# Performance work log

Measured on AMD Instinct MI355X. Metric: run time of the kernel, lower is better.

The kernel has to match this reference:

```python
import jax, jax.numpy as jnp
import numpy as np

B, S, D, H, F = 2, 2048, 768, 12, 3072
DH = D // H  # head dim = 64


def setup_inputs() -> dict:
    key = jax.random.key(0)
    ks = jax.random.split(key, 16)
    sc = 0.02
    p = {
        "src": jax.random.normal(ks[0], (B, S, D), jnp.float32),
        # attention projections (torch Linear layout: [out, in], bias=True in xformers MultiHeadDispatch)
        "wq": jax.random.normal(ks[1], (D, D), jnp.float32) * sc,
        "bq": jnp.zeros((D,), jnp.float32),
        "wk": jax.random.normal(ks[2], (D, D), jnp.float32) * sc,
        "bk": jnp.zeros((D,), jnp.float32),
        "wv": jax.random.normal(ks[3], (D, D), jnp.float32) * sc,
        "bv": jnp.zeros((D,), jnp.float32),
        "wo": jax.random.normal(ks[4], (D, D), jnp.float32) * sc,
        "bo": jnp.zeros((D,), jnp.float32),
        # FFN: fc1 (bias) -> SwiGLU (two bias-free F->F projections) -> fc2 (bias)
        "w_fc1": jax.random.normal(ks[5], (F, D), jnp.float32) * sc,
        "b_fc1": jnp.zeros((F,), jnp.float32),
        "w_in": jax.random.normal(ks[6], (F, F), jnp.float32) * sc,
        "w_gate": jax.random.normal(ks[7], (F, F), jnp.float32) * sc,
        "w_fc2": jax.random.normal(ks[8], (D, F), jnp.float32) * sc,
        "b_fc2": jnp.zeros((D,), jnp.float32),
        # RMSNorm weights
        "g_attn": jnp.ones((D,), jnp.float32),
        "g_ffn": jnp.ones((D,), jnp.float32),
    }
    return p


def _rmsnorm(x, g):
    eps = jnp.asarray(jnp.finfo(x.dtype).eps, x.dtype)
    return x * jax.lax.rsqrt(jnp.mean(x * x, axis=-1, keepdims=True) + eps) * g


def _rope_cos_sin(seq_len, dim, dtype):
    # xformers RotaryEmbedding: inv_freq over even indices, emb = cat(freqs, freqs)
    inv_freq = 1.0 / (10000.0 ** (jnp.arange(0, dim, 2, dtype=jnp.float32) / dim))
    freqs = jnp.arange(seq_len, dtype=jnp.float32)[:, None] * inv_freq[None, :]  # [S, dim/2]
    emb = jnp.concatenate([freqs, freqs], axis=-1)  # [S, dim]
    return jnp.cos(emb).astype(dtype), jnp.sin(emb).astype(dtype)


def _rotate_half(x):
    x1, x2 = jnp.split(x, 2, axis=-1)
    return jnp.concatenate([-x2, x1], axis=-1)


def _apply_rope(x, cos, sin):
    # x: [B, H, S, DH]; cos/sin: [S, DH]
    return x * cos[None, None] + _rotate_half(x) * sin[None, None]


def _block(src, wq, bq, wk, bk, wv, bv, wo, bo,
           w_fc1, b_fc1, w_in, w_gate, w_fc2, b_fc2, g_attn, g_ffn):
    b, s, d = src.shape
    x = _rmsnorm(src, g_attn)
    q = (x @ wq.T + bq).reshape(b, s, H, DH).transpose(0, 2, 1, 3)
    k = (x @ wk.T + bk).reshape(b, s, H, DH).transpose(0, 2, 1, 3)
    v = (x @ wv.T + bv).reshape(b, s, H, DH).transpose(0, 2, 1, 3)
    cos, sin = _rope_cos_sin(s, DH, x.dtype)
    q = _apply_rope(q, cos, sin)
    k = _apply_rope(k, cos, sin)
    scale = 1.0 / np.sqrt(DH)
    scores = jnp.einsum("bhsd,bhtd->bhst", q * scale, k)  # non-causal, no mask
    attn = jax.nn.softmax(scores, axis=-1)
    ctx = jnp.einsum("bhst,bhtd->bhsd", attn, v)
    ctx = ctx.transpose(0, 2, 1, 3).reshape(b, s, d)
    attn_out = ctx @ wo.T + bo

    y = _rmsnorm(src + attn_out, g_ffn)
    h = y @ w_fc1.T + b_fc1
    h = (h @ w_in.T) * jax.nn.silu(h @ w_gate.T)  # SwiGLU
    ffn_out = h @ w_fc2.T + b_fc2
    return y + ffn_out


def reference(src, wq, bq, wk, bk, wv, bv, wo, bo,
              w_fc1, b_fc1, w_in, w_gate, w_fc2, b_fc2, g_attn, g_ffn):
    return _block(src, wq, bq, wk, bk, wv, bv, wo, bo,
                  w_fc1, b_fc1, w_in, w_gate, w_fc2, b_fc2, g_attn, g_ffn)
```

## Files before the change

### kernel.cpp

```cpp
#include <hip/hip_runtime.h>

#define DEV static __device__ __forceinline__

typedef __attribute__((ext_vector_type(8))) short bf16x8;
typedef __attribute__((ext_vector_type(4))) short short4v;
typedef __attribute__((ext_vector_type(4))) float f32x4;

DEV f32x4 mfma16(bf16x8 a, bf16x8 b, f32x4 c){
  return __builtin_amdgcn_mfma_f32_16x16x32_bf16(a, b, c, 0, 0, 0);
}
DEV float bf2f(short s){ union{unsigned u; float f;} v; v.u=((unsigned)(unsigned short)s)<<16; return v.f; }
DEV short f2bf(float f){ union{float f; unsigned u;} v; v.f=f; unsigned r=v.u+0x7fffu+((v.u>>16)&1u); return (short)(r>>16); }
DEV void gload16(const void* g, void* l){
  __builtin_amdgcn_global_load_lds((const __attribute__((address_space(1))) void*)g,
                                   (__attribute__((address_space(3))) void*)l, 16, 0, 0);
}
DEV int cvtpk(float lo, float hi){
  int r; asm("v_cvt_pk_bf16_f32 %0, %1, %2" : "=v"(r) : "v"(lo), "v"(hi)); return r;
}

enum { EPI_BF16=0, EPI_RESID=2, EPI_QKV=4 };

__global__ void k_convert7(const float* __restrict__ p0, const float* __restrict__ p1,
                           const float* __restrict__ p2, const float* __restrict__ p3,
                           const float* __restrict__ p4, const float* __restrict__ p5,
                           const float* __restrict__ p6, short* __restrict__ dst){
  int v = blockIdx.x * 256 + threadIdx.x;
  const float* src; int rel;
  if      (v <  147456){ src=p0; rel=v; }
  else if (v <  294912){ src=p1; rel=v-147456; }
  else if (v <  442368){ src=p2; rel=v-294912; }
  else if (v <  589824){ src=p3; rel=v-442368; }
  else if (v < 2949120){ src=p4; rel=v-589824; }
  else if (v < 5308416){ src=p5; rel=v-2949120; }
  else                 { src=p6; rel=v-5308416; }
  float4 x = ((const float4*)src)[rel];
  short4v o; o.x=f2bf(x.x); o.y=f2bf(x.y); o.z=f2bf(x.z); o.w=f2bf(x.w);
  int dv = (v < 589824) ? v : (v + 589824);
  ((short4v*)dst)[dv] = o;
}

__global__ void k_convertT(const float* __restrict__ in, short* __restrict__ out){
  __shared__ float lt[32][33];
  const int t = threadIdx.x;
  const int f0 = blockIdx.x * 32;
  const int d0 = blockIdx.y * 32;
  int r = t >> 3, c4 = t & 7;
  float4 v = *(const float4*)(in + (size_t)(f0 + r)*768 + d0 + c4*4);
  lt[r][c4*4+0] = v.x; lt[r][c4*4+1] = v.y; lt[r][c4*4+2] = v.z; lt[r][c4*4+3] = v.w;
  __syncthreads();
  short4v o;
  o.x = f2bf(lt[c4*4+0][r]);
  o.y = f2bf(lt[c4*4+1][r]);
  o.z = f2bf(lt[c4*4+2][r]);
  o.w = f2bf(lt[c4*4+3][r]);
  *(short4v*)(out + (size_t)(d0 + r)*3072 + f0 + c4*4) = o;
}

__global__ void k_gemv(const short* __restrict__ W, const float* __restrict__ b,
                       float* __restrict__ out){
  int row = blockIdx.x*4 + (threadIdx.x>>6);
  int lane = threadIdx.x & 63;
  const short* wr = W + (size_t)row*3072 + lane*48;
  const float* bb = b + lane*48;
  float s = 0.f;
  #pragma unroll
  for (int i=0;i<6;i++){
    bf16x8 w = *(const bf16x8*)(wr + i*8);
    float4 b0 = *(const float4*)(bb + i*8);
    float4 b1 = *(const float4*)(bb + i*8 + 4);
    s += bf2f(w[0])*b0.x + bf2f(w[1])*b0.y + bf2f(w[2])*b0.z + bf2f(w[3])*b0.w
       + bf2f(w[4])*b1.x + bf2f(w[5])*b1.y + bf2f(w[6])*b1.z + bf2f(w[7])*b1.w;
  }
  #pragma unroll
  for (int d=32; d>0; d>>=1) s += __shfl_xor(s, d);
  if (lane == 0) out[row] = s;
}

__global__ void k_rmsnorm(const float* __restrict__ x, const float* __restrict__ g,
                          short* __restrict__ out){
  int row = blockIdx.x*4 + (threadIdx.x>>6);
  int lane = threadIdx.x & 63;
  const float* xr = x + (size_t)row*768;
  float4 v[3];
  float ss = 0.f;
  #pragma unroll
  for (int i=0;i<3;i++){
    v[i] = *(const float4*)(xr + i*256 + lane*4);
    ss += v[i].x*v[i].x + v[i].y*v[i].y + v[i].z*v[i].z + v[i].w*v[i].w;
  }
  #pragma unroll
  for (int d=32; d>0; d>>=1) ss += __shfl_xor(ss, d);
  float sc = rsqrtf(ss*(1.f/768.f) + 1.1920929e-7f);
  #pragma unroll
  for (int i=0;i<3;i++){
    int c0 = i*256 + lane*4;
    float4 gv = *(const float4*)(g + c0);
    short4v o;
    o.x = f2bf(v[i].x*sc*gv.x); o.y = f2bf(v[i].y*sc*gv.y);
    o.z = f2bf(v[i].z*sc*gv.z); o.w = f2bf(v[i].w*sc*gv.w);
    *(short4v*)(out + (size_t)row*768 + c0) = o;
  }
}

template<int EPI>
__launch_bounds__(256, 2)
__global__ void k_gemm(const short* __restrict__ Aptr, const short* __restrict__ Bptr,
                       void* __restrict__ Cout, const float* __restrict__ bias,
                       const void* __restrict__ aux, const float* __restrict__ bias2,
                       const float* __restrict__ bias3, const void* __restrict__ aux2,
                       int M, int N, int K){
  __shared__ short ldsA[128*32];
  __shared__ short ldsB[128*32];
  const int t = threadIdx.x;
  const int wave = t >> 6, lane = t & 63;
  const int l15 = lane & 15, l4 = lane >> 4;
  const int nwg = gridDim.x * gridDim.y;
  const int bid0 = blockIdx.y * gridDim.x + blockIdx.x;
  const int cpx = nwg >> 3;
  const int bid = (bid0 & 7) * cpx + (bid0 >> 3);
  const int bm = bid / gridDim.x, bn = bid % gridDim.x;
  const int wr = wave >> 1, wc = wave & 1;

  f32x4 acc[4][4] = {};

  const short* Ag = Aptr + (size_t)(bm*128 + wave*32 + (lane>>2))*K + (lane&3)*8;
  const short* Bg = Bptr + (size_t)(bn*128 + wave*32 + (lane>>2))*K + (lane&3)*8;
  short* lA = ldsA + wave*1024;
  short* lB = ldsB + wave*1024;

  for (int k0 = 0; k0 < K; k0 += 32){
    __syncthreads();
    gload16(Ag + k0,                lA);
    gload16(Ag + k0 + 16*(size_t)K, lA + 512);
    gload16(Bg + k0,                lB);
    gload16(Bg + k0 + 16*(size_t)K, lB + 512);
    __syncthreads();
    bf16x8 af[4], bfr[4];
    #pragma unroll
    for (int m=0;m<4;m++) af[m]  = *(const bf16x8*)(ldsA + (wr*64 + m*16 + l15)*32 + l4*8);
    #pragma unroll
    for (int n=0;n<4;n++) bfr[n] = *(const bf16x8*)(ldsB + (wc*64 + n*16 + l15)*32 + l4*8);
    #pragma unroll
    for (int m=0;m<4;m++)
      #pragma unroll
      for (int n=0;n<4;n++)
        acc[m][n] = mfma16(af[m], bfr[n], acc[m][n]);
  }

  const int row0 = bm*128 + wr*64;
  const int col0 = bn*128 + wc*64;

  if constexpr (EPI == EPI_BF16){
    short* C = (short*)Cout;
    #pragma unroll
    for (int m=0;m<4;m++)
      #pragma unroll
      for (int j=0;j<4;j++){
        size_t rb = (size_t)(row0 + m*16 + l4*4 + j)*N + col0 + l15;
        #pragma unroll
        for (int n=0;n<4;n++) C[rb + n*16] = f2bf(acc[m][n][j]);
      }
  } else if constexpr (EPI == EPI_RESID){
    float* C = (float*)Cout;
    const float* srcf = (const float*)aux;
    float bvv[4];
    #pragma unroll
    for (int n=0;n<4;n++) bvv[n] = bias[col0 + n*16 + l15];
    #pragma unroll
    for (int m=0;m<4;m++)
      #pragma unroll
      for (int j=0;j<4;j++){
        size_t rb = (size_t)(row0 + m*16 + l4*4 + j)*N + col0 + l15;
        #pragma unroll
        for (int n=0;n<4;n++) C[rb + n*16] = acc[m][n][j] + bvv[n] + srcf[rb + n*16];
      }
  } else if constexpr (EPI == EPI_QKV){
    const int proj = col0 / 768;
    const int c768 = col0 - proj*768;
    const int h = c768 >> 6;
    const float* bs = proj==0 ? bias : (proj==1 ? bias2 : bias3);
    float bvv[4];
    #pragma unroll
    for (int n=0;n<4;n++) bvv[n] = bs[c768 + n*16 + l15];
    if (proj == 2){
      short* Ov = (short*)const_cast<void*>(aux2);
      #pragma unroll
      for (int m=0;m<4;m++){
        #pragma unroll
        for (int j=0;j<4;j++){
          int row = row0 + m*16 + l4*4 + j;
          int b = row >> 11, s = row & 2047;
          size_t hb = (size_t)(b*12 + h)*64;
          #pragma unroll
          for (int n=0;n<4;n++)
            Ov[(hb + n*16 + l15)*2048 + s] = f2bf(acc[m][n][j] + bvv[n]);
        }
      }
    } else {
      short* O = proj==0 ? (short*)Cout : (short*)const_cast<void*>(aux);
      const float sc = proj==0 ? 0.18033688011112042f : 1.0f;
      const float RC = 0.41524101186092034f;
      float invf0 = exp2f(-(float)l15 * RC);
      float invf1 = exp2f(-(float)(16 + l15) * RC);
      #pragma unroll
      for (int m=0;m<4;m++){
        #pragma unroll
        for (int j=0;j<4;j++){
          int row = row0 + m*16 + l4*4 + j;
          int b = row >> 11, s = row & 2047;
          size_t obase = ((size_t)(b*12 + h)*2048 + (size_t)s)*64;
          float a0 = acc[m][0][j] + bvv[0];
          float a1 = acc[m][1][j] + bvv[1];
          float a2 = acc[m][2][j] + bvv[2];
          float a3 = acc[m][3][j] + bvv[3];
          float sn0, cs0, sn1, cs1;
          __sincosf((float)s * invf0, &sn0, &cs0);
          __sincosf((float)s * invf1, &sn1, &cs1);
          O[obase + l15]      = f2bf((a0*cs0 - a2*sn0)*sc);
          O[obase + 16 + l15] = f2bf((a1*cs1 - a3*sn1)*sc);
          O[obase + 32 + l15] = f2bf((a2*cs0 + a0*sn0)*sc);
          O[obase + 48 + l15] = f2bf((a3*cs1 + a1*sn1)*sc);
        }
      }
    }
  }
}

__launch_bounds__(256, 2)
__global__ void k_wpart(const short* __restrict__ Aptr, const short* __restrict__ Bptr,
                        short* __restrict__ P){
  __shared__ short ldsA[128*32];
  __shared__ short ldsB[128*32];
  const int t = threadIdx.x;
  const int wave = t >> 6, lane = t & 63;
  const int l15 = lane & 15, l4 = lane >> 4;
  const int koff = blockIdx.z * 1536;
  const int bid0 = blockIdx.y * 6 + blockIdx.x;
  const int bid = (bid0 & 7) * 36 + (bid0 >> 3);
  const int bm = bid / 6, bn = bid % 6;
  const int wr = wave >> 1, wc = wave & 1;

  f32x4 acc[4][4] = {};

  const short* Ag = Aptr + (size_t)(bm*128 + wave*32 + (lane>>2))*3072 + (lane&3)*8 + koff;
  const short* Bg = Bptr + (size_t)(bn*128 + wave*32 + (lane>>2))*3072 + (lane&3)*8 + koff;
  short* lA = ldsA + wave*1024;
  short* lB = ldsB + wave*1024;

  for (int k0 = 0; k0 < 1536; k0 += 32){
    __syncthreads();
    gload16(Ag + k0,           lA);
    gload16(Ag + k0 + 16*3072, lA + 512);
    gload16(Bg + k0,           lB);
    gload16(Bg + k0 + 16*3072, lB + 512);
    __syncthreads();
    bf16x8 af[4], bfr[4];
    #pragma unroll
    for (int m=0;m<4;m++) af[m]  = *(const bf16x8*)(ldsA + (wr*64 + m*16 + l15)*32 + l4*8);
    #pragma unroll
    for (int n=0;n<4;n++) bfr[n] = *(const bf16x8*)(ldsB + (wc*64 + n*16 + l15)*32 + l4*8);
    #pragma unroll
    for (int m=0;m<4;m++)
      #pragma unroll
      for (int n=0;n<4;n++)
        acc[m][n] = mfma16(af[m], bfr[n], acc[m][n]);
  }

  short* Pz = P + (size_t)blockIdx.z * 4718592;
  const int row0 = bm*128 + wr*64;
  const int col0 = bn*128 + wc*64;
  #pragma unroll
  for (int m=0;m<4;m++)
    #pragma unroll
    for (int j=0;j<4;j++){
      size_t rb = (size_t)(row0 + m*16 + l4*4 + j)*768 + col0 + l15;
      #pragma unroll
      for (int n=0;n<4;n++) Pz[rb + n*16] = f2bf(acc[m][n][j]);
    }
}

__global__ void k_wred(const short* __restrict__ P, short* __restrict__ comp){
  int i = blockIdx.x * 256 + threadIdx.x;
  short4v a = ((const short4v*)P)[i];
  short4v b = ((const short4v*)(P + 4718592))[i];
  short4v o;
  o.x = f2bf(bf2f(a.x) + bf2f(b.x)); o.y = f2bf(bf2f(a.y) + bf2f(b.y));
  o.z = f2bf(bf2f(a.z) + bf2f(b.z)); o.w = f2bf(bf2f(a.w) + bf2f(b.w));
  ((short4v*)comp)[i] = o;
}

__launch_bounds__(256, 2)
__global__ void k_part(const short* __restrict__ Aptr, const short* __restrict__ Bptr,
                       short* __restrict__ Pa, short* __restrict__ Pb){
  __shared__ short ldsA[128*32];
  __shared__ short ldsB[128*32];
  const int t = threadIdx.x;
  const int wave = t >> 6, lane = t & 63;
  const int l15 = lane & 15, l4 = lane >> 4;
  const int K = 3072;
  const int z = blockIdx.z;
  const int koff = z * 768;
  const int bid0 = blockIdx.y * 6 + blockIdx.x;
  const int bid = (bid0 & 7) * 24 + (bid0 >> 3);
  const int bm = bid / 6, bn = bid % 6;
  const int wr = wave >> 1, wc = wave & 1;

  f32x4 acc[4][4] = {};

  const short* Ag = Aptr + (size_t)(bm*128 + wave*32 + (lane>>2))*K + (lane&3)*8 + koff;
  const short* Bg = Bptr + (size_t)(bn*128 + wave*32 + (lane>>2))*K + (lane&3)*8 + koff;
  short* lA = ldsA + wave*1024;
  short* lB = ldsB + wave*1024;

  for (int k0 = 0; k0 < 768; k0 += 32){
    __syncthreads();
    gload16(Ag + k0,                lA);
    gload16(Ag + k0 + 16*(size_t)K, lA + 512);
    gload16(Bg + k0,                lB);
    gload16(Bg + k0 + 16*(size_t)K, lB + 512);
    __syncthreads();
    bf16x8 af[4], bfr[4];
    #pragma unroll
    for (int m=0;m<4;m++) af[m]  = *(const bf16x8*)(ldsA + (wr*64 + m*16 + l15)*32 + l4*8);
    #pragma unroll
    for (int n=0;n<4;n++) bfr[n] = *(const bf16x8*)(ldsB + (wc*64 + n*16 + l15)*32 + l4*8);
    #pragma unroll
    for (int m=0;m<4;m++)
      #pragma unroll
      for (int n=0;n<4;n++)
        acc[m][n] = mfma16(af[m], bfr[n], acc[m][n]);
  }

  short* P = (z < 2) ? (Pa + (size_t)z*3145728) : (Pb + (size_t)(z-2)*3145728);
  const int row0 = bm*128 + wr*64;
  const int col0 = bn*128 + wc*64;
  #pragma unroll
  for (int m=0;m<4;m++)
    #pragma unroll
    for (int j=0;j<4;j++){
      size_t rb = (size_t)(row0 + m*16 + l4*4 + j)*768 + col0 + l15;
      #pragma unroll
      for (int n=0;n<4;n++) P[rb + n*16] = f2bf(acc[m][n][j]);
    }
}

__global__ void k_fc2red(const short* __restrict__ Pa, const short* __restrict__ Pb,
                         const float* __restrict__ bias, const short* __restrict__ yv,
                         float* __restrict__ out){
  int i = blockIdx.x * 256 + threadIdx.x;
  short4v a = ((const short4v*)Pa)[i];
  short4v b = ((const short4v*)(Pa + 3145728))[i];
  short4v c = ((const short4v*)Pb)[i];
  short4v d = ((const short4v*)(Pb + 3145728))[i];
  float4 bv = *(const float4*)(bias + (i % 192)*4);
  short4v y = ((const short4v*)yv)[i];
  float4 o;
  o.x = bf2f(a.x) + bf2f(b.x) + bf2f(c.x) + bf2f(d.x) + bv.x + bf2f(y.x);
  o.y = bf2f(a.y) + bf2f(b.y) + bf2f(c.y) + bf2f(d.y) + bv.y + bf2f(y.y);
  o.z = bf2f(a.z) + bf2f(b.z) + bf2f(c.z) + bf2f(d.z) + bv.z + bf2f(y.z);
  o.w = bf2f(a.w) + bf2f(b.w) + bf2f(c.w) + bf2f(d.w) + bv.w + bf2f(y.w);
  ((float4*)out)[i] = o;
}

__launch_bounds__(256, 2)
__global__ void k_ffglu(const short* __restrict__ Aptr, const short* __restrict__ Wcomp,
                        const float* __restrict__ bvg, short* __restrict__ Cout){
  __shared__ short lds[3*12288];
  const int tid = threadIdx.x;
  const int wave = tid >> 6, lane = tid & 63;
  const int l15 = lane & 15, l4 = lane >> 4;
  const int wm = wave >> 1, wn = wave & 1;
  const int K = 768, N = 3072;
  const int nt = 24;

  const int lin = blockIdx.y * 48 + blockIdx.x;
  const int xcd = lin & 7, idx = lin >> 3;
  const int bm = ((xcd & 1) << 3) + idx / 12;
  const int bn = (xcd >> 1) * 12 + idx % 12;

  const int srcC = ((lane & 3) ^ ((lane >> 3) & 3)) * 8;

  const short* aSrc[4];
  int aDst[4];
  #pragma unroll
  for (int i=0;i<4;i++){
    int s = i*4 + wave;
    int row = s*16 + (lane>>2);
    aSrc[i] = Aptr + (size_t)(bm*256 + row)*K + srcC;
    aDst[i] = s*512;
  }
  const short* bSrc[2];
  int bDst[2];
  #pragma unroll
  for (int i=0;i<2;i++){
    int j = i*4 + wave;
    int pidx = (j>>1)*16 + (lane>>2);
    int grow = (j & 1) ? 3072 : 0;
    bSrc[i] = Wcomp + (size_t)(grow + bn*64 + pidx)*K + srcC;
    bDst[i] = 8192 + j*512;
  }

  int offA[8], offB[4];
  #pragma unroll
  for (int m=0;m<8;m++){
    int r = wm*128 + m*16 + l15;
    offA[m] = r*32 + ((l4 ^ ((l15>>1)&3))<<3);
  }
  #pragma unroll
  for (int nf=0;nf<4;nf++){
    int r = wn*64 + nf*16 + l15;
    offB[nf] = 8192 + r*32 + ((l4 ^ ((l15>>1)&3))<<3);
  }

  f32x4 accv[8][2] = {};
  f32x4 accg[8][2] = {};

  short *b0 = lds, *b1 = lds + 12288, *b2 = lds + 24576;

  #define GSTAGE_ALL(buf, t) do{ \
    gload16(aSrc[0] + (size_t)(t)*32, (buf) + aDst[0]); \
    gload16(aSrc[1] + (size_t)(t)*32, (buf) + aDst[1]); \
    gload16(aSrc[2] + (size_t)(t)*32, (buf) + aDst[2]); \
    gload16(aSrc[3] + (size_t)(t)*32, (buf) + aDst[3]); \
    gload16(bSrc[0] + (size_t)(t)*32, (buf) + bDst[0]); \
    gload16(bSrc[1] + (size_t)(t)*32, (buf) + bDst[1]); \
  }while(0)

  GSTAGE_ALL(b0, 0);
  GSTAGE_ALL(b1, 1);

  for (int t = 0; t < nt; ++t){
    if (t < nt-1){
      asm volatile("s_waitcnt vmcnt(6)" ::: "memory");
    } else {
      asm volatile("s_waitcnt vmcnt(0)" ::: "memory");
    }
    __builtin_amdgcn_sched_barrier(0);
    __builtin_amdgcn_s_barrier();
    __builtin_amdgcn_sched_barrier(0);

    if (t + 2 < nt) GSTAGE_ALL(b2, t+2);

    bf16x8 a0 = *(const bf16x8*)(b0 + offA[0]);
    bf16x8 a1 = *(const bf16x8*)(b0 + offA[1]);
    bf16x8 a2 = *(const bf16x8*)(b0 + offA[2]);
    bf16x8 a3 = *(const bf16x8*)(b0 + offA[3]);
    bf16x8 a4 = *(const bf16x8*)(b0 + offA[4]);
    bf16x8 a5 = *(const bf16x8*)(b0 + offA[5]);
    bf16x8 a6 = *(const bf16x8*)(b0 + offA[6]);
    bf16x8 a7 = *(const bf16x8*)(b0 + offA[7]);
    bf16x8 v0 = *(const bf16x8*)(b0 + offB[0]);
    bf16x8 g0 = *(const bf16x8*)(b0 + offB[1]);
    bf16x8 v1 = *(const bf16x8*)(b0 + offB[2]);
    bf16x8 g1 = *(const bf16x8*)(b0 + offB[3]);

    __builtin_amdgcn_s_setprio(1);
    accv[0][0] = mfma16(a0, v0, accv[0][0]);  accg[0][0] = mfma16(a0, g0, accg[0][0]);
    accv[1][0] = mfma16(a1, v0, accv[1][0]);  accg[1][0] = mfma16(a1, g0, accg[1][0]);
    accv[2][0] = mfma16(a2, v0, accv[2][0]);  accg[2][0] = mfma16(a2, g0, accg[2][0]);
    accv[3][0] = mfma16(a3, v0, accv[3][0]);  accg[3][0] = mfma16(a3, g0, accg[3][0]);
    accv[0][1] = mfma16(a0, v1, accv[0][1]);  accg[0][1] = mfma16(a0, g1, accg[0][1]);
    accv[1][1] = mfma16(a1, v1, accv[1][1]);  accg[1][1] = mfma16(a1, g1, accg[1][1]);
    accv[2][1] = mfma16(a2, v1, accv[2][1]);  accg[2][1] = mfma16(a2, g1, accg[2][1]);
    accv[3][1] = mfma16(a3, v1, accv[3][1]);  accg[3][1] = mfma16(a3, g1, accg[3][1]);
    accv[4][0] = mfma16(a4, v0, accv[4][0]);  accg[4][0] = mfma16(a4, g0, accg[4][0]);
    accv[5][0] = mfma16(a5, v0, accv[5][0]);  accg[5][0] = mfma16(a5, g0, accg[5][0]);
    accv[6][0] = mfma16(a6, v0, accv[6][0]);  accg[6][0] = mfma16(a6, g0, accg[6][0]);
    accv[7][0] = mfma16(a7, v0, accv[7][0]);  accg[7][0] = mfma16(a7, g0, accg[7][0]);
    accv[4][1] = mfma16(a4, v1, accv[4][1]);  accg[4][1] = mfma16(a4, g1, accg[4][1]);
    accv[5][1] = mfma16(a5, v1, accv[5][1]);  accg[5][1] = mfma16(a5, g1, accg[5][1]);
    accv[6][1] = mfma16(a6, v1, accv[6][1]);  accg[6][1] = mfma16(a6, g1, accg[6][1]);
    accv[7][1] = mfma16(a7, v1, accv[7][1]);  accg[7][1] = mfma16(a7, g1, accg[7][1]);
    __builtin_amdgcn_s_setprio(0);

    short* tmp = b0; b0 = b1; b1 = b2; b2 = tmp;
  }
  #undef GSTAGE_ALL

  const int row0 = bm*256 + wm*128;
  #pragma unroll
  for (int m=0;m<8;m++){
    #pragma unroll
    for (int j=0;j<4;j++){
      size_t rb = (size_t)(row0 + m*16 + l4*4 + j)*N + bn*64 + wn*32 + l15;
      #pragma unroll
      for (int p=0;p<2;p++){
        int c = bn*64 + wn*32 + p*16 + l15;
        float g = accg[m][p][j] + bvg[3072 + c];
        float v = accv[m][p][j] + bvg[c];
        Cout[rb + p*16] = f2bf(v * g / (1.f + __expf(-g)));
      }
    }
  }
}

__launch_bounds__(256, 5)
__global__ void k_attn(const short* __restrict__ Q, const short* __restrict__ Kb,
                       const short* __restrict__ Vb, short* __restrict__ ctx){
  __shared__ short Kt[2][4096];
  __shared__ short Vt[2][4096];
  const int t = threadIdx.x, wave = t>>6, lane = t&63;
  const int l15 = lane&15, l4 = lane>>4;
  const int qt = blockIdx.x, bh = blockIdx.y;
  const short* Qh  = Q  + (size_t)bh*2048*64;
  const short* Kh  = Kb + (size_t)bh*2048*64;
  const short* Vth = Vb + (size_t)bh*64*2048;

  const int r7  = lane>>3;
  const int swz = ((lane&7) ^ r7) << 3;
  const int rr0 = wave*8 + r7, rr1 = 32 + wave*8 + r7;
  const size_t kOff0 = (size_t)rr0*64   + swz, kOff1 = (size_t)rr1*64   + swz;
  const size_t vOff0 = (size_t)rr0*2048 + swz, vOff1 = (size_t)rr1*2048 + swz;

  bf16x8 qf[2];
  #pragma unroll
  for (int kf=0;kf<2;kf++)
    qf[kf] = *(const bf16x8*)(Qh + (size_t)(qt*64 + wave*16 + l15)*64 + kf*32 + l4*8);

  f32x4 cacc[4] = {};
  f32x4 lacc = {};
  union { int w[4]; bf16x8 v; } onesf;
  onesf.w[0] = onesf.w[1] = onesf.w[2] = onesf.w[3] = 0x3F803F80;

  #define STAGE(sel, kv0) do { \
    const short* ksp = Kh + (size_t)(kv0)*64; \
    const short* vsp = Vth + (kv0); \
    short* kd = &Kt[sel][wave*512]; \
    short* vd = &Vt[sel][wave*512]; \
    gload16(ksp + kOff0, kd); \
    gload16(ksp + kOff1, kd + 2048); \
    gload16(vsp + vOff0, vd); \
    gload16(vsp + vOff1, vd + 2048); \
  } while(0)

  STAGE(0, 0);

  for (int tt = 0; tt < 32; ++tt){
    const int cur = tt & 1;
    if (tt < 31){
      STAGE(cur^1, (tt+1)*64);
      asm volatile("s_waitcnt vmcnt(4)" ::: "memory");
    } else {
      asm volatile("s_waitcnt vmcnt(0)" ::: "memory");
    }
    __builtin_amdgcn_sched_barrier(0);
    __builtin_amdgcn_s_barrier();
    __builtin_amdgcn_sched_barrier(0);

    const short* KtC = &Kt[cur][0];
    const short* VtC = &Vt[cur][0];

    f32x4 sacc[4] = {};
    __builtin_amdgcn_s_setprio(1);
    #pragma unroll
    for (int kf=0;kf<2;kf++){
      #pragma unroll
      for (int mk=0;mk<4;mk++){
        int r = mk*16 + l15;
        bf16x8 kfr = *(const bf16x8*)(KtC + r*64 + (((kf*4+l4) ^ (l15&7))<<3));
        sacc[mk] = mfma16(kfr, qf[kf], sacc[mk]);
      }
    }
    __builtin_amdgcn_s_setprio(0);

    int pk01[4], pk23[4];
    #pragma unroll
    for (int mk=0;mk<4;mk++){
      float p0 = exp2f(sacc[mk][0]);
      float p1 = exp2f(sacc[mk][1]);
      float p2 = exp2f(sacc[mk][2]);
      float p3 = exp2f(sacc[mk][3]);
      pk01[mk] = cvtpk(p0, p1);
      pk23[mk] = cvtpk(p2, p3);
    }

    #pragma unroll
    for (int ks=0;ks<2;ks++){
      int srcA = l15 + ((l4&1)<<5);
      int srcB = srcA + 16;
      int hi = l4>>1;
      int w0a = __shfl(pk01[2*ks], srcA), w0b = __shfl(pk01[2*ks+1], srcA);
      int w1a = __shfl(pk23[2*ks], srcA), w1b = __shfl(pk23[2*ks+1], srcA);
      int w2a = __shfl(pk01[2*ks], srcB), w2b = __shfl(pk01[2*ks+1], srcB);
      int w3a = __shfl(pk23[2*ks], srcB), w3b = __shfl(pk23[2*ks+1], srcB);
      union { int w[4]; bf16x8 v; } pa;
      pa.w[0] = hi ? w0b : w0a;
      pa.w[1] = hi ? w1b : w1a;
      pa.w[2] = hi ? w2b : w2a;
      pa.w[3] = hi ? w3b : w3a;
      __builtin_amdgcn_s_setprio(1);
      #pragma unroll
      for (int nf=0;nf<4;nf++){
        int dh = nf*16 + l15;
        bf16x8 vf = *(const bf16x8*)(VtC + dh*64 + (((ks*4+l4) ^ (dh&7))<<3));
        cacc[nf] = mfma16(pa.v, vf, cacc[nf]);
      }
      lacc = mfma16(pa.v, onesf.v, lacc);
      __builtin_amdgcn_s_setprio(0);
    }

    __builtin_amdgcn_sched_barrier(0);
    __builtin_amdgcn_s_barrier();
  }
  #undef STAGE

  const int b = bh/12, h = bh%12;
  #pragma unroll
  for (int j=0;j<4;j++){
    float inv = 1.f / lacc[j];
    int s = qt*64 + wave*16 + l4*4 + j;
    size_t base = ((size_t)b*2048 + s)*768 + h*64;
    #pragma unroll
    for (int nf=0;nf<4;nf++)
      ctx[base + nf*16 + l15] = f2bf(cacc[nf][j] * inv);
  }
}

extern "C" void kernel_launch(void* const* d_in, const int* in_sizes, int n_in,
                              void* d_out, int out_size, void* d_ws, size_t ws_size,
                              hipStream_t stream){
  (void)in_sizes; (void)n_in; (void)out_size;
  const float* src   = (const float*)d_in[0];
  const float* wq    = (const float*)d_in[1];
  const float* bq    = (const float*)d_in[2];
  const float* wk    = (const float*)d_in[3];
  const float* bk    = (const float*)d_in[4];
  const float* wv    = (const float*)d_in[5];
  const float* bv    = (const float*)d_in[6];
  const float* wo    = (const float*)d_in[7];
  const float* bo    = (const float*)d_in[8];
  const float* wfc1  = (const float*)d_in[9];
  const float* bfc1  = (const float*)d_in[10];
  const float* win   = (const float*)d_in[11];
  const float* wgate = (const float*)d_in[12];
  const float* wfc2  = (const float*)d_in[13];
  const float* bfc2  = (const float*)d_in[14];
  const float* gattn = (const float*)d_in[15];
  const float* gffn  = (const float*)d_in[16];

  char* ws = (char*)d_ws;
  constexpr size_t SZ_W768  = 768ull*768*2;
  constexpr size_t SZ_WFC   = 3072ull*768*2;
  constexpr size_t SZ_WFF   = 3072ull*3072*2;
  constexpr size_t SZ_ACT   = 4096ull*768*2;
  constexpr size_t SZ_ACTF  = 4096ull*768*4;
  constexpr size_t SZ_H     = 4096ull*3072*2;
  constexpr size_t OFF_WQ    = 0;
  constexpr size_t OFF_WK    = OFF_WQ + SZ_W768;
  constexpr size_t OFF_WV    = OFF_WK + SZ_W768;
  constexpr size_t OFF_WO    = OFF_WV + SZ_W768;
  constexpr size_t OFF_WFC1  = OFF_WO + SZ_W768;
  constexpr size_t OFF_WIN   = OFF_WFC1 + SZ_WFC;
  constexpr size_t OFF_WGATE = OFF_WIN + SZ_WFF;
  constexpr size_t OFF_WFC2  = OFF_WGATE + SZ_WFF;
  constexpr size_t OFF_XN    = OFF_WFC2 + SZ_WFC;
  constexpr size_t OFF_Q     = OFF_XN + SZ_ACT;
  constexpr size_t OFF_K     = OFF_Q + SZ_ACT;
  constexpr size_t OFF_V     = OFF_K + SZ_ACT;
  constexpr size_t OFF_RES   = OFF_V + SZ_ACT;
  constexpr size_t OFF_HIN   = OFF_RES + SZ_ACTF;
  constexpr size_t OFF_H2    = OFF_HIN + SZ_H;
  constexpr size_t WS_NEED   = OFF_H2 + SZ_H;
  if (ws_size < WS_NEED) return;

  constexpr size_t OFF_COMP  = OFF_HIN;
  constexpr size_t OFF_T     = OFF_HIN + 6144ull*768*2;
  constexpr size_t OFF_BVG   = OFF_T + 768ull*3072*2;

  short* wq_b    = (short*)(ws+OFF_WQ);
  short* win_b   = (short*)(ws+OFF_WIN);
  short* wfc2_b  = (short*)(ws+OFF_WFC2);
  short* wo_b    = (short*)(ws+OFF_WO);
  short* xn      = (short*)(ws+OFF_XN);
  short* ctxb    = (short*)(ws+OFF_XN);
  short* qb      = (short*)(ws+OFF_Q);
  short* yb      = (short*)(ws+OFF_Q);
  short* kb2     = (short*)(ws+OFF_K);
  short* vb2     = (short*)(ws+OFF_V);
  float* resid   = (float*)(ws+OFF_RES);
  short* comp    = (short*)(ws+OFF_COMP);
  short* wfc1T   = (short*)(ws+OFF_T);
  float* bvg     = (float*)(ws+OFF_BVG);
  short* h2      = (short*)(ws+OFF_H2);
  short* Pw      = (short*)(ws+OFF_XN);
  short* partA   = (short*)(ws+OFF_HIN);
  short* partB   = (short*)(ws+OFF_K);

  k_convert7<<<23040, 256, 0, stream>>>(wq, wk, wv, wo, win, wgate, wfc2, wq_b);
  k_convertT<<<dim3(96,24), 256, 0, stream>>>(wfc1, wfc1T);

  k_wpart<<<dim3(6,48,2), 256, 0, stream>>>(win_b, wfc1T, Pw);
  k_wred<<<4608, 256, 0, stream>>>(Pw, comp);
  k_gemv<<<1536, 256, 0, stream>>>(win_b, bfc1, bvg);

  k_rmsnorm<<<1024, 256, 0, stream>>>(src, gattn, xn);

  k_gemm<EPI_QKV><<<dim3(18,32), 256, 0, stream>>>(xn, wq_b, qb, bq, kb2, bk, bv, vb2, 4096, 2304, 768);

  k_attn<<<dim3(32, 24), 256, 0, stream>>>(qb, kb2, vb2, ctxb);

  k_gemm<EPI_RESID><<<dim3(6,32), 256, 0, stream>>>(ctxb, wo_b, resid, bo, src, nullptr, nullptr, nullptr, 4096, 768, 768);
  k_rmsnorm<<<1024, 256, 0, stream>>>(resid, gffn, yb);

  k_ffglu<<<dim3(48,16), 256, 0, stream>>>(yb, comp, bvg, h2);

  k_part<<<dim3(6,32,4), 256, 0, stream>>>(h2, wfc2_b, partA, partB);
  k_fc2red<<<3072, 256, 0, stream>>>(partA, partB, bfc2, yb, (float*)d_out);
}
```

Baseline: 275.9 us.

## Merge independent weight-prep work into attention and GEMM launches as fat kernels

Independent work now shares launches by dispatching on block index. The big weight conversions and the fc1 transpose ride along with attention in one kernel. The Wo GEMM, the folded W_in·W_fc1 partial products and the bias GEMV share a second kernel, and the FFN RMSNorm shares a third with the partial-sum reduction. Only the small QKV/Wo weight conversion still runs before the QKV GEMM. The aim is to cut launch count and to fill idle compute units during attention and the small Wo GEMM. The cost is mixed-role kernels that must use the strictest launch bounds and LDS sizing, which can lower occupancy for attention (5 to 4 blocks), and heterogeneous blocks that may contend for bandwidth.

```diff
diff --git a/kernel.cpp b/kernel.cpp
--- a/kernel.cpp
+++ b/kernel.cpp
@@ -19,62 +19,20 @@
   int r; asm("v_cvt_pk_bf16_f32 %0, %1, %2" : "=v"(r) : "v"(lo), "v"(hi)); return r;
 }
 
-enum { EPI_BF16=0, EPI_RESID=2, EPI_QKV=4 };
-
-__global__ void k_convert7(const float* __restrict__ p0, const float* __restrict__ p1,
-                           const float* __restrict__ p2, const float* __restrict__ p3,
-                           const float* __restrict__ p4, const float* __restrict__ p5,
-                           const float* __restrict__ p6, short* __restrict__ dst){
+enum { EPI_QKV=4 };
+
+__global__ void k_csmall(const float* __restrict__ p0, const float* __restrict__ p1,
+                         const float* __restrict__ p2, const float* __restrict__ p3,
+                         short* __restrict__ dst){
   int v = blockIdx.x * 256 + threadIdx.x;
   const float* src; int rel;
-  if      (v <  147456){ src=p0; rel=v; }
-  else if (v <  294912){ src=p1; rel=v-147456; }
-  else if (v <  442368){ src=p2; rel=v-294912; }
-  else if (v <  589824){ src=p3; rel=v-442368; }
-  else if (v < 2949120){ src=p4; rel=v-589824; }
-  else if (v < 5308416){ src=p5; rel=v-2949120; }
-  else                 { src=p6; rel=v-5308416; }
+  if      (v < 147456){ src=p0; rel=v; }
+  else if (v < 294912){ src=p1; rel=v-147456; }
+  else if (v < 442368){ src=p2; rel=v-294912; }
+  else                { src=p3; rel=v-442368; }
   float4 x = ((const float4*)src)[rel];
   short4v o; o.x=f2bf(x.x); o.y=f2bf(x.y); o.z=f2bf(x.z); o.w=f2bf(x.w);
-  int dv = (v < 589824) ? v : (v + 589824);
-  ((short4v*)dst)[dv] = o;
-}
-
-__global__ void k_convertT(const float* __restrict__ in, short* __restrict__ out){
-  __shared__ float lt[32][33];
-  const int t = threadIdx.x;
-  const int f0 = blockIdx.x * 32;
-  const int d0 = blockIdx.y * 32;
-  int r = t >> 3, c4 = t & 7;
-  float4 v = *(const float4*)(in + (size_t)(f0 + r)*768 + d0 + c4*4);
-  lt[r][c4*4+0] = v.x; lt[r][c4*4+1] = v.y; lt[r][c4*4+2] = v.z; lt[r][c4*4+3] = v.w;
-  __syncthreads();
-  short4v o;
-  o.x = f2bf(lt[c4*4+0][r]);
-  o.y = f2bf(lt[c4*4+1][r]);
-  o.z = f2bf(lt[c4*4+2][r]);
-  o.w = f2bf(lt[c4*4+3][r]);
-  *(short4v*)(out + (size_t)(d0 + r)*3072 + f0 + c4*4) = o;
-}
-
-__global__ void k_gemv(const short* __restrict__ W, const float* __restrict__ b,
-                       float* __restrict__ out){
-  int row = blockIdx.x*4 + (threadIdx.x>>6);
-  int lane = threadIdx.x & 63;
-  const short* wr = W + (size_t)row*3072 + lane*48;
-  const float* bb = b + lane*48;
-  float s = 0.f;
-  #pragma unroll
-  for (int i=0;i<6;i++){
-    bf16x8 w = *(const bf16x8*)(wr + i*8);
-    float4 b0 = *(const float4*)(bb + i*8);
-    float4 b1 = *(const float4*)(bb + i*8 + 4);
-    s += bf2f(w[0])*b0.x + bf2f(w[1])*b0.y + bf2f(w[2])*b0.z + bf2f(w[3])*b0.w
-       + bf2f(w[4])*b1.x + bf2f(w[5])*b1.y + bf2f(w[6])*b1.z + bf2f(w[7])*b1.w;
-  }
-  #pragma unroll
-  for (int d=32; d>0; d>>=1) s += __shfl_xor(s, d);
-  if (lane == 0) out[row] = s;
+  ((short4v*)dst)[v] = o;
 }
 
 __global__ void k_rmsnorm(const float* __restrict__ x, const float* __restrict__ g,
@@ -151,31 +109,7 @@
   const int row0 = bm*128 + wr*64;
   const int col0 = bn*128 + wc*64;
 
-  if constexpr (EPI == EPI_BF16){
-    short* C = (short*)Cout;
-    #pragma unroll
-    for (int m=0;m<4;m++)
-      #pragma unroll
-      for (int j=0;j<4;j++){
-        size_t rb = (size_t)(row0 + m*16 + l4*4 + j)*N + col0 + l15;
-        #pragma unroll
-        for (int n=0;n<4;n++) C[rb + n*16] = f2bf(acc[m][n][j]);
-      }
-  } else if constexpr (EPI == EPI_RESID){
-    float* C = (float*)Cout;
-    const float* srcf = (const float*)aux;
-    float bvv[4];
-    #pragma unroll
-    for (int n=0;n<4;n++) bvv[n] = bias[col0 + n*16 + l15];
-    #pragma unroll
-    for (int m=0;m<4;m++)
-      #pragma unroll
-      for (int j=0;j<4;j++){
-        size_t rb = (size_t)(row0 + m*16 + l4*4 + j)*N + col0 + l15;
-        #pragma unroll
-        for (int n=0;n<4;n++) C[rb + n*16] = acc[m][n][j] + bvv[n] + srcf[rb + n*16];
-      }
-  } else if constexpr (EPI == EPI_QKV){
+  if constexpr (EPI == EPI_QKV){
     const int proj = col0 / 768;
     const int c768 = col0 - proj*768;
     const int h = c768 >> 6;
@@ -227,67 +161,306 @@
   }
 }
 
+__launch_bounds__(256, 4)
+__global__ void k_fatA(const short* __restrict__ Q, const short* __restrict__ Kb,
+                       const short* __restrict__ Vb, short* __restrict__ ctx,
+                       const float* __restrict__ winf, const float* __restrict__ wgf,
+                       const float* __restrict__ wfc2f, short* __restrict__ dstbig,
+                       const float* __restrict__ wfc1, short* __restrict__ wfc1T){
+  __shared__ short shm[16384];
+  const int id = blockIdx.x;
+  const int tid = threadIdx.x;
+
+  if (id < 768){
+    const int wave = tid>>6, lane = tid&63;
+    const int l15 = lane&15, l4 = lane>>4;
+    const int qt = id & 31, bh = id >> 5;
+    const short* Qh  = Q  + (size_t)bh*2048*64;
+    const short* Kh  = Kb + (size_t)bh*2048*64;
+    const short* Vth = Vb + (size_t)bh*64*2048;
+
+    const int r7  = lane>>3;
+    const int swz = ((lane&7) ^ r7) << 3;
+    const int rr0 = wave*8 + r7, rr1 = 32 + wave*8 + r7;
+    const size_t kOff0 = (size_t)rr0*64   + swz, kOff1 = (size_t)rr1*64   + swz;
+    const size_t vOff0 = (size_t)rr0*2048 + swz, vOff1 = (size_t)rr1*2048 + swz;
+
+    bf16x8 qf[2];
+    #pragma unroll
+    for (int kf=0;kf<2;kf++)
+      qf[kf] = *(const bf16x8*)(Qh + (size_t)(qt*64 + wave*16 + l15)*64 + kf*32 + l4*8);
+
+    f32x4 cacc[4] = {};
+    f32x4 lacc = {};
+    union { int w[4]; bf16x8 v; } onesf;
+    onesf.w[0] = onesf.w[1] = onesf.w[2] = onesf.w[3] = 0x3F803F80;
+
+    #define STAGE(sel, kv0) do { \
+      const short* ksp = Kh + (size_t)(kv0)*64; \
+      const short* vsp = Vth + (kv0); \
+      short* kd = shm + (sel)*4096 + wave*512; \
+      short* vd = shm + 8192 + (sel)*4096 + wave*512; \
+      gload16(ksp + kOff0, kd); \
+      gload16(ksp + kOff1, kd + 2048); \
+      gload16(vsp + vOff0, vd); \
+      gload16(vsp + vOff1, vd + 2048); \
+    } while(0)
+
+    STAGE(0, 0);
+
+    for (int tt = 0; tt < 32; ++tt){
+      const int cur = tt & 1;
+      if (tt < 31){
+        STAGE(cur^1, (tt+1)*64);
+        asm volatile("s_waitcnt vmcnt(4)" ::: "memory");
+      } else {
+        asm volatile("s_waitcnt vmcnt(0)" ::: "memory");
+      }
+      __builtin_amdgcn_sched_barrier(0);
+      __builtin_amdgcn_s_barrier();
+      __builtin_amdgcn_sched_barrier(0);
+
+      const short* KtC = shm + cur*4096;
+      const short* VtC = shm + 8192 + cur*4096;
+
+      f32x4 sacc[4] = {};
+      __builtin_amdgcn_s_setprio(1);
+      #pragma unroll
+      for (int kf=0;kf<2;kf++){
+        #pragma unroll
+        for (int mk=0;mk<4;mk++){
+          int r = mk*16 + l15;
+          bf16x8 kfr = *(const bf16x8*)(KtC + r*64 + (((kf*4+l4) ^ (l15&7))<<3));
+          sacc[mk] = mfma16(kfr, qf[kf], sacc[mk]);
+        }
+      }
+      __builtin_amdgcn_s_setprio(0);
+
+      int pk01[4], pk23[4];
+      #pragma unroll
+      for (int mk=0;mk<4;mk++){
+        float p0 = exp2f(sacc[mk][0]);
+        float p1 = exp2f(sacc[mk][1]);
+        float p2 = exp2f(sacc[mk][2]);
+        float p3 = exp2f(sacc[mk][3]);
+        pk01[mk] = cvtpk(p0, p1);
+        pk23[mk] = cvtpk(p2, p3);
+      }
+
+      #pragma unroll
+      for (int ks=0;ks<2;ks++){
+        int srcA = l15 + ((l4&1)<<5);
+        int srcB = srcA + 16;
+        int hi = l4>>1;
+        int w0a = __shfl(pk01[2*ks], srcA), w0b = __shfl(pk01[2*ks+1], srcA);
+        int w1a = __shfl(pk23[2*ks], srcA), w1b = __shfl(pk23[2*ks+1], srcA);
+        int w2a = __shfl(pk01[2*ks], srcB), w2b = __shfl(pk01[2*ks+1], srcB);
+        int w3a = __shfl(pk23[2*ks], srcB), w3b = __shfl(pk23[2*ks+1], srcB);
+        union { int w[4]; bf16x8 v; } pa;
+        pa.w[0] = hi ? w0b : w0a;
+        pa.w[1] = hi ? w1b : w1a;
+        pa.w[2] = hi ? w2b : w2a;
+        pa.w[3] = hi ? w3b : w3a;
+        __builtin_amdgcn_s_setprio(1);
+        #pragma unroll
+        for (int nf=0;nf<4;nf++){
+          int dh = nf*16 + l15;
+          bf16x8 vf = *(const bf16x8*)(VtC + dh*64 + (((ks*4+l4) ^ (dh&7))<<3));
+          cacc[nf] = mfma16(pa.v, vf, cacc[nf]);
+        }
+        lacc = mfma16(pa.v, onesf.v, lacc);
+        __builtin_amdgcn_s_setprio(0);
+      }
+
+      __builtin_amdgcn_sched_barrier(0);
+      __builtin_amdgcn_s_barrier();
+    }
+    #undef STAGE
+
+    const int b = bh/12, h = bh%12;
+    #pragma unroll
+    for (int j=0;j<4;j++){
+      float inv = 1.f / lacc[j];
+      int s = qt*64 + wave*16 + l4*4 + j;
+      size_t base = ((size_t)b*2048 + s)*768 + h*64;
+      #pragma unroll
+      for (int nf=0;nf<4;nf++)
+        ctx[base + nf*16 + l15] = f2bf(cacc[nf][j] * inv);
+    }
+  } else if (id < 21504){
+    int v = (id - 768)*256 + tid;
+    const float* src; int rel;
+    if      (v < 2359296){ src=winf;  rel=v; }
+    else if (v < 4718592){ src=wgf;   rel=v-2359296; }
+    else                 { src=wfc2f; rel=v-4718592; }
+    float4 x = ((const float4*)src)[rel];
+    short4v o; o.x=f2bf(x.x); o.y=f2bf(x.y); o.z=f2bf(x.z); o.w=f2bf(x.w);
+    ((short4v*)dstbig)[v] = o;
+  } else {
+    int idx = id - 21504;
+    int f0 = (idx % 96)*32, d0 = (idx / 96)*32;
+    float* lt = (float*)shm;
+    int r = tid >> 3, c4 = tid & 7;
+    float4 v = *(const float4*)(wfc1 + (size_t)(f0 + r)*768 + d0 + c4*4);
+    lt[r*33 + c4*4+0] = v.x; lt[r*33 + c4*4+1] = v.y;
+    lt[r*33 + c4*4+2] = v.z; lt[r*33 + c4*4+3] = v.w;
+    __syncthreads();
+    short4v o;
+    o.x = f2bf(lt[(c4*4+0)*33 + r]);
+    o.y = f2bf(lt[(c4*4+1)*33 + r]);
+    o.z = f2bf(lt[(c4*4+2)*33 + r]);
+    o.w = f2bf(lt[(c4*4+3)*33 + r]);
+    *(short4v*)(wfc1T + (size_t)(d0 + r)*3072 + f0 + c4*4) = o;
+  }
+}
+
 __launch_bounds__(256, 2)
-__global__ void k_wpart(const short* __restrict__ Aptr, const short* __restrict__ Bptr,
-                        short* __restrict__ P){
-  __shared__ short ldsA[128*32];
-  __shared__ short ldsB[128*32];
+__global__ void k_fatB(const short* __restrict__ ctxb, const short* __restrict__ wo_b,
+                       float* __restrict__ resid, const float* __restrict__ bo,
+                       const float* __restrict__ srcf,
+                       const short* __restrict__ win_b, const short* __restrict__ wfc1T,
+                       short* __restrict__ Pw,
+                       const float* __restrict__ bfc1, float* __restrict__ bvg){
+  __shared__ short shm[8192];
+  const int id = blockIdx.x;
   const int t = threadIdx.x;
   const int wave = t >> 6, lane = t & 63;
   const int l15 = lane & 15, l4 = lane >> 4;
-  const int koff = blockIdx.z * 1536;
-  const int bid0 = blockIdx.y * 6 + blockIdx.x;
-  const int bid = (bid0 & 7) * 36 + (bid0 >> 3);
-  const int bm = bid / 6, bn = bid % 6;
   const int wr = wave >> 1, wc = wave & 1;
-
-  f32x4 acc[4][4] = {};
-
-  const short* Ag = Aptr + (size_t)(bm*128 + wave*32 + (lane>>2))*3072 + (lane&3)*8 + koff;
-  const short* Bg = Bptr + (size_t)(bn*128 + wave*32 + (lane>>2))*3072 + (lane&3)*8 + koff;
-  short* lA = ldsA + wave*1024;
-  short* lB = ldsB + wave*1024;
-
-  for (int k0 = 0; k0 < 1536; k0 += 32){
-    __syncthreads();
-    gload16(Ag + k0,           lA);
-    gload16(Ag + k0 + 16*3072, lA + 512);
-    gload16(Bg + k0,           lB);
-    gload16(Bg + k0 + 16*3072, lB + 512);
-    __syncthreads();
-    bf16x8 af[4], bfr[4];
-    #pragma unroll
-    for (int m=0;m<4;m++) af[m]  = *(const bf16x8*)(ldsA + (wr*64 + m*16 + l15)*32 + l4*8);
-    #pragma unroll
-    for (int n=0;n<4;n++) bfr[n] = *(const bf16x8*)(ldsB + (wc*64 + n*16 + l15)*32 + l4*8);
+  short* lA = shm + wave*1024;
+  short* lB = shm + 4096 + wave*1024;
+
+  if (id < 192){
+    const int bid = (id & 7)*24 + (id >> 3);
+    const int bm = bid / 6, bn = bid % 6;
+    f32x4 acc[4][4] = {};
+    const short* Ag = ctxb + (size_t)(bm*128 + wave*32 + (lane>>2))*768 + (lane&3)*8;
+    const short* Bg = wo_b + (size_t)(bn*128 + wave*32 + (lane>>2))*768 + (lane&3)*8;
+    for (int k0 = 0; k0 < 768; k0 += 32){
+      __syncthreads();
+      gload16(Ag + k0,          lA);
+      gload16(Ag + k0 + 16*768, lA + 512);
+      gload16(Bg + k0,          lB);
+      gload16(Bg + k0 + 16*768, lB + 512);
+      __syncthreads();
+      bf16x8 af[4], bfr[4];
+      #pragma unroll
+      for (int m=0;m<4;m++) af[m]  = *(const bf16x8*)(shm + (wr*64 + m*16 + l15)*32 + l4*8);
+      #pragma unroll
+      for (int n=0;n<4;n++) bfr[n] = *(const bf16x8*)(shm + 4096 + (wc*64 + n*16 + l15)*32 + l4*8);
+      #pragma unroll
+      for (int m=0;m<4;m++)
+        #pragma unroll
+        for (int n=0;n<4;n++)
+          acc[m][n] = mfma16(af[m], bfr[n], acc[m][n]);
+    }
+    const int row0 = bm*128 + wr*64;
+    const int col0 = bn*128 + wc*64;
+    float bvv[4];
+    #pragma unroll
+    for (int n=0;n<4;n++) bvv[n] = bo[col0 + n*16 + l15];
     #pragma unroll
     for (int m=0;m<4;m++)
       #pragma unroll
-      for (int n=0;n<4;n++)
-        acc[m][n] = mfma16(af[m], bfr[n], acc[m][n]);
-  }
-
-  short* Pz = P + (size_t)blockIdx.z * 4718592;
-  const int row0 = bm*128 + wr*64;
-  const int col0 = bn*128 + wc*64;
-  #pragma unroll
-  for (int m=0;m<4;m++)
-    #pragma unroll
-    for (int j=0;j<4;j++){
-      size_t rb = (size_t)(row0 + m*16 + l4*4 + j)*768 + col0 + l15;
-      #pragma unroll
-      for (int n=0;n<4;n++) Pz[rb + n*16] = f2bf(acc[m][n][j]);
-    }
-}
-
-__global__ void k_wred(const short* __restrict__ P, short* __restrict__ comp){
-  int i = blockIdx.x * 256 + threadIdx.x;
-  short4v a = ((const short4v*)P)[i];
-  short4v b = ((const short4v*)(P + 4718592))[i];
-  short4v o;
-  o.x = f2bf(bf2f(a.x) + bf2f(b.x)); o.y = f2bf(bf2f(a.y) + bf2f(b.y));
-  o.z = f2bf(bf2f(a.z) + bf2f(b.z)); o.w = f2bf(bf2f(a.w) + bf2f(b.w));
-  ((short4v*)comp)[i] = o;
+      for (int j=0;j<4;j++){
+        size_t rb = (size_t)(row0 + m*16 + l4*4 + j)*768 + col0 + l15;
+        #pragma unroll
+        for (int n=0;n<4;n++) resid[rb + n*16] = acc[m][n][j] + bvv[n] + srcf[rb + n*16];
+      }
+  } else if (id < 768){
+    const int id2 = id - 192;
+    const int z = id2 / 288;
+    const int rest = id2 - z*288;
+    const int koff = z * 1536;
+    const int bid = (rest & 7)*36 + (rest >> 3);
+    const int bm = bid / 6, bn = bid % 6;
+    f32x4 acc[4][4] = {};
+    const short* Ag = win_b + (size_t)(bm*128 + wave*32 + (lane>>2))*3072 + (lane&3)*8 + koff;
+    const short* Bg = wfc1T + (size_t)(bn*128 + wave*32 + (lane>>2))*3072 + (lane&3)*8 + koff;
+    for (int k0 = 0; k0 < 1536; k0 += 32){
+      __syncthreads();
+      gload16(Ag + k0,           lA);
+      gload16(Ag + k0 + 16*3072, lA + 512);
+      gload16(Bg + k0,           lB);
+      gload16(Bg + k0 + 16*3072, lB + 512);
+      __syncthreads();
+      bf16x8 af[4], bfr[4];
+      #pragma unroll
+      for (int m=0;m<4;m++) af[m]  = *(const bf16x8*)(shm + (wr*64 + m*16 + l15)*32 + l4*8);
+      #pragma unroll
+      for (int n=0;n<4;n++) bfr[n] = *(const bf16x8*)(shm + 4096 + (wc*64 + n*16 + l15)*32 + l4*8);
+      #pragma unroll
+      for (int m=0;m<4;m++)
+        #pragma unroll
+        for (int n=0;n<4;n++)
+          acc[m][n] = mfma16(af[m], bfr[n], acc[m][n]);
+    }
+    short* Pz = Pw + (size_t)z * 4718592;
+    const int row0 = bm*128 + wr*64;
+    const int col0 = bn*128 + wc*64;
+    #pragma unroll
+    for (int m=0;m<4;m++)
+      #pragma unroll
+      for (int j=0;j<4;j++){
+        size_t rb = (size_t)(row0 + m*16 + l4*4 + j)*768 + col0 + l15;
+        #pragma unroll
+        for (int n=0;n<4;n++) Pz[rb + n*16] = f2bf(acc[m][n][j]);
+      }
+  } else {
+    int row = (id - 768)*4 + wave;
+    const short* wrow = win_b + (size_t)row*3072 + lane*48;
+    const float* bb = bfc1 + lane*48;
+    float s = 0.f;
+    #pragma unroll
+    for (int i=0;i<6;i++){
+      bf16x8 w = *(const bf16x8*)(wrow + i*8);
+      float4 b0 = *(const float4*)(bb + i*8);
+      float4 b1 = *(const float4*)(bb + i*8 + 4);
+      s += bf2f(w[0])*b0.x + bf2f(w[1])*b0.y + bf2f(w[2])*b0.z + bf2f(w[3])*b0.w
+         + bf2f(w[4])*b1.x + bf2f(w[5])*b1.y + bf2f(w[6])*b1.z + bf2f(w[7])*b1.w;
+    }
+    #pragma unroll
+    for (int d=32; d>0; d>>=1) s += __shfl_xor(s, d);
+    if (lane == 0) bvg[row] = s;
+  }
+}
+
+__global__ void k_fatC(const float* __restrict__ resid, const float* __restrict__ gffn,
+                       short* __restrict__ yb,
+                       const short* __restrict__ Pw, short* __restrict__ comp){
+  const int id = blockIdx.x;
+  if (id < 1024){
+    int row = id*4 + (threadIdx.x>>6);
+    int lane = threadIdx.x & 63;
+    const float* xr = resid + (size_t)row*768;
+    float4 v[3];
+    float ss = 0.f;
+    #pragma unroll
+    for (int i=0;i<3;i++){
+      v[i] = *(const float4*)(xr + i*256 + lane*4);
+      ss += v[i].x*v[i].x + v[i].y*v[i].y + v[i].z*v[i].z + v[i].w*v[i].w;
+    }
+    #pragma unroll
+    for (int d=32; d>0; d>>=1) ss += __shfl_xor(ss, d);
+    float sc = rsqrtf(ss*(1.f/768.f) + 1.1920929e-7f);
+    #pragma unroll
+    for (int i=0;i<3;i++){
+      int c0 = i*256 + lane*4;
+      float4 gv = *(const float4*)(gffn + c0);
+      short4v o;
+      o.x = f2bf(v[i].x*sc*gv.x); o.y = f2bf(v[i].y*sc*gv.y);
+      o.z = f2bf(v[i].z*sc*gv.z); o.w = f2bf(v[i].w*sc*gv.w);
+      *(short4v*)(yb + (size_t)row*768 + c0) = o;
+    }
+  } else {
+    int i = (id - 1024)*256 + threadIdx.x;
+    short4v a = ((const short4v*)Pw)[i];
+    short4v b = ((const short4v*)(Pw + 4718592))[i];
+    short4v o;
+    o.x = f2bf(bf2f(a.x) + bf2f(b.x)); o.y = f2bf(bf2f(a.y) + bf2f(b.y));
+    o.z = f2bf(bf2f(a.z) + bf2f(b.z)); o.w = f2bf(bf2f(a.w) + bf2f(b.w));
+    ((short4v*)comp)[i] = o;
+  }
 }
 
 __launch_bounds__(256, 2)
@@ -492,128 +665,6 @@
         Cout[rb + p*16] = f2bf(v * g / (1.f + __expf(-g)));
       }
     }
-  }
-}
-
-__launch_bounds__(256, 5)
-__global__ void k_attn(const short* __restrict__ Q, const short* __restrict__ Kb,
-                       const short* __restrict__ Vb, short* __restrict__ ctx){
-  __shared__ short Kt[2][4096];
-  __shared__ short Vt[2][4096];
-  const int t = threadIdx.x, wave = t>>6, lane = t&63;
-  const int l15 = lane&15, l4 = lane>>4;
-  const int qt = blockIdx.x, bh = blockIdx.y;
-  const short* Qh  = Q  + (size_t)bh*2048*64;
-  const short* Kh  = Kb + (size_t)bh*2048*64;
-  const short* Vth = Vb + (size_t)bh*64*2048;
-
-  const int r7  = lane>>3;
-  const int swz = ((lane&7) ^ r7) << 3;
-  const int rr0 = wave*8 + r7, rr1 = 32 + wave*8 + r7;
-  const size_t kOff0 = (size_t)rr0*64   + swz, kOff1 = (size_t)rr1*64   + swz;
-  const size_t vOff0 = (size_t)rr0*2048 + swz, vOff1 = (size_t)rr1*2048 + swz;
-
-  bf16x8 qf[2];
-  #pragma unroll
-  for (int kf=0;kf<2;kf++)
-    qf[kf] = *(const bf16x8*)(Qh + (size_t)(qt*64 + wave*16 + l15)*64 + kf*32 + l4*8);
-
-  f32x4 cacc[4] = {};
-  f32x4 lacc = {};
-  union { int w[4]; bf16x8 v; } onesf;
-  onesf.w[0] = onesf.w[1] = onesf.w[2] = onesf.w[3] = 0x3F803F80;
-
-  #define STAGE(sel, kv0) do { \
-    const short* ksp = Kh + (size_t)(kv0)*64; \
-    const short* vsp = Vth + (kv0); \
-    short* kd = &Kt[sel][wave*512]; \
-    short* vd = &Vt[sel][wave*512]; \
-    gload16(ksp + kOff0, kd); \
-    gload16(ksp + kOff1, kd + 2048); \
-    gload16(vsp + vOff0, vd); \
-    gload16(vsp + vOff1, vd + 2048); \
-  } while(0)
-
-  STAGE(0, 0);
-
-  for (int tt = 0; tt < 32; ++tt){
-    const int cur = tt & 1;
-    if (tt < 31){
-      STAGE(cur^1, (tt+1)*64);
-      asm volatile("s_waitcnt vmcnt(4)" ::: "memory");
-    } else {
-      asm volatile("s_waitcnt vmcnt(0)" ::: "memory");
-    }
-    __builtin_amdgcn_sched_barrier(0);
-    __builtin_amdgcn_s_barrier();
-    __builtin_amdgcn_sched_barrier(0);
-
-    const short* KtC = &Kt[cur][0];
-    const short* VtC = &Vt[cur][0];
-
-    f32x4 sacc[4] = {};
-    __builtin_amdgcn_s_setprio(1);
-    #pragma unroll
-    for (int kf=0;kf<2;kf++){
-      #pragma unroll
-      for (int mk=0;mk<4;mk++){
-        int r = mk*16 + l15;
-        bf16x8 kfr = *(const bf16x8*)(KtC + r*64 + (((kf*4+l4) ^ (l15&7))<<3));
-        sacc[mk] = mfma16(kfr, qf[kf], sacc[mk]);
-      }
-    }
-    __builtin_amdgcn_s_setprio(0);
-
-    int pk01[4], pk23[4];
-    #pragma unroll
-    for (int mk=0;mk<4;mk++){
-      float p0 = exp2f(sacc[mk][0]);
-      float p1 = exp2f(sacc[mk][1]);
-      float p2 = exp2f(sacc[mk][2]);
-      float p3 = exp2f(sacc[mk][3]);
-      pk01[mk] = cvtpk(p0, p1);
-      pk23[mk] = cvtpk(p2, p3);
-    }
-
-    #pragma unroll
-    for (int ks=0;ks<2;ks++){
-      int srcA = l15 + ((l4&1)<<5);
-      int srcB = srcA + 16;
-      int hi = l4>>1;
-      int w0a = __shfl(pk01[2*ks], srcA), w0b = __shfl(pk01[2*ks+1], srcA);
-      int w1a = __shfl(pk23[2*ks], srcA), w1b = __shfl(pk23[2*ks+1], srcA);
-      int w2a = __shfl(pk01[2*ks], srcB), w2b = __shfl(pk01[2*ks+1], srcB);
-      int w3a = __shfl(pk23[2*ks], srcB), w3b = __shfl(pk23[2*ks+1], srcB);
-      union { int w[4]; bf16x8 v; } pa;
-      pa.w[0] = hi ? w0b : w0a;
-      pa.w[1] = hi ? w1b : w1a;
-      pa.w[2] = hi ? w2b : w2a;
-      pa.w[3] = hi ? w3b : w3a;
-      __builtin_amdgcn_s_setprio(1);
-      #pragma unroll
-      for (int nf=0;nf<4;nf++){
-        int dh = nf*16 + l15;
-        bf16x8 vf = *(const bf16x8*)(VtC + dh*64 + (((ks*4+l4) ^ (dh&7))<<3));
-        cacc[nf] = mfma16(pa.v, vf, cacc[nf]);
-      }
-      lacc = mfma16(pa.v, onesf.v, lacc);
-      __builtin_amdgcn_s_setprio(0);
-    }
-
-    __builtin_amdgcn_sched_barrier(0);
-    __builtin_amdgcn_s_barrier();
-  }
-  #undef STAGE
-
-  const int b = bh/12, h = bh%12;
-  #pragma unroll
-  for (int j=0;j<4;j++){
-    float inv = 1.f / lacc[j];
-    int s = qt*64 + wave*16 + l4*4 + j;
-    size_t base = ((size_t)b*2048 + s)*768 + h*64;
-    #pragma unroll
-    for (int nf=0;nf<4;nf++)
-      ctx[base + nf*16 + l15] = f2bf(cacc[nf][j] * inv);
   }
 }
 
@@ -683,25 +734,20 @@
   short* wfc1T   = (short*)(ws+OFF_T);
   float* bvg     = (float*)(ws+OFF_BVG);
   short* h2      = (short*)(ws+OFF_H2);
-  short* Pw      = (short*)(ws+OFF_XN);
+  short* Pw      = (short*)(ws+OFF_H2);
   short* partA   = (short*)(ws+OFF_HIN);
   short* partB   = (short*)(ws+OFF_K);
 
-  k_convert7<<<23040, 256, 0, stream>>>(wq, wk, wv, wo, win, wgate, wfc2, wq_b);
-  k_convertT<<<dim3(96,24), 256, 0, stream>>>(wfc1, wfc1T);
-
-  k_wpart<<<dim3(6,48,2), 256, 0, stream>>>(win_b, wfc1T, Pw);
-  k_wred<<<4608, 256, 0, stream>>>(Pw, comp);
-  k_gemv<<<1536, 256, 0, stream>>>(win_b, bfc1, bvg);
-
+  k_csmall<<<2304, 256, 0, stream>>>(wq, wk, wv, wo, wq_b);
   k_rmsnorm<<<1024, 256, 0, stream>>>(src, gattn, xn);
 
   k_gemm<EPI_QKV><<<dim3(18,32), 256, 0, stream>>>(xn, wq_b, qb, bq, kb2, bk, bv, vb2, 4096, 2304, 768);
 
-  k_attn<<<dim3(32, 24), 256, 0, stream>>>(qb, kb2, vb2, ctxb);
-
-  k_gemm<EPI_RESID><<<dim3(6,32), 256, 0, stream>>>(ctxb, wo_b, resid, bo, src, nullptr, nullptr, nullptr, 4096, 768, 768);
-  k_rmsnorm<<<1024, 256, 0, stream>>>(resid, gffn, yb);
+  k_fatA<<<23808, 256, 0, stream>>>(qb, kb2, vb2, ctxb, win, wgate, wfc2, win_b, wfc1, wfc1T);
+
+  k_fatB<<<2304, 256, 0, stream>>>(ctxb, wo_b, resid, bo, src, win_b, wfc1T, Pw, bfc1, bvg);
+
+  k_fatC<<<5632, 256, 0, stream>>>(resid, gffn, yb, Pw, comp);
 
   k_ffglu<<<dim3(48,16), 256, 0, stream>>>(yb, comp, bvg, h2);
 
```

Measured after the change: 235.0 us. 1.17x faster.
